# Kernel tuning notes

Measured on AMD Instinct MI355X. Metric: run time of the kernel, lower is better.

Reference implementation:

```python
import jax, jax.numpy as jnp
import numpy as np
import math

# --- delta-LFIT rule-space combinatorics ---
NUM_VARS, DELAYS = 3, 3
N = NUM_VARS * DELAYS  # 9 delayed variables

def delta_count(l, n):
    # number of rule bodies of length exactly l: choose l of n vars, each with a polarity
    return math.comb(n, l) * (2 ** l)

MAX_RULE_LEN = max(delta_count(l, N) for l in range(N + 1))  # 5376
OUT_DIM = MAX_RULE_LEN + 1  # padded logits + trailing 'empty rule' logit
N_HEADS = N + 1  # rules_pred has heads for rule_len = 0..N

B, S = 512, 1
DIM_IN = 1024
DIM_HIDDEN = 1024
LAYERS = 4  # -> LAYERS+1 Linear layers total (no nonlinearity in the original Sequential)


def setup_inputs() -> dict:
    key = jax.random.key(0)
    ks = jax.random.split(key, 4)
    latent = jax.random.normal(ks[0], (B, S, DIM_IN), dtype=jnp.float32)
    rule_len = jax.random.randint(ks[1], (B,), 0, N_HEADS, dtype=jnp.int32)

    n_lin = LAYERS + 1  # dim_in==dim_hidden so all trunk linears stack uniformly
    scale = 1.0 / np.sqrt(DIM_HIDDEN)
    W_mlp = jax.random.normal(ks[2], (n_lin, DIM_HIDDEN, DIM_HIDDEN), dtype=jnp.float32) * scale
    b_mlp = jnp.zeros((n_lin, DIM_HIDDEN), dtype=jnp.float32)

    # Padded head weight bank: row layout matches torch.cat((out[..., :-1], zeros_pad, out[..., -1:]))
    rng = np.random.default_rng(0)
    Wh = np.zeros((N_HEADS, OUT_DIM, DIM_HIDDEN), dtype=np.float32)
    bh = np.zeros((N_HEADS, OUT_DIM), dtype=np.float32)
    for l in range(N_HEADS):
        d = delta_count(l, N) + 1  # head l output dim: length(l)-length(l-1)+1
        w = (rng.standard_normal((d, DIM_HIDDEN)) * scale).astype(np.float32)
        b = (rng.standard_normal(d) * 0.01).astype(np.float32)
        Wh[l, : d - 1] = w[:-1]
        Wh[l, OUT_DIM - 1] = w[-1]
        bh[l, : d - 1] = b[:-1]
        bh[l, OUT_DIM - 1] = b[-1]

    return {
        "latent": latent,
        "W_mlp": W_mlp,
        "b_mlp": b_mlp,
        "W_heads": jnp.asarray(Wh),
        "b_heads": jnp.asarray(bh),
        "rule_len": rule_len,
    }


def reference(latent, W_mlp, b_mlp, W_heads, b_heads, rule_len):
    # Trunk: stack of Linear layers, no activation (matches the original Sequential)
    h = latent  # [B, S, H]
    for i in range(W_mlp.shape[0]):
        h = h @ W_mlp[i].T + b_mlp[i]
    # Per-sample dynamic head dispatch (rule_len_is_diff=True branch), vectorized:
    # compute all padded heads, then gather each sample's head.
    all_out = jnp.einsum('bsh,loh->bslo', h, W_heads) + b_heads  # [B, S, N_HEADS, OUT_DIM]
    idx = rule_len.astype(jnp.int32)[:, None, None, None]  # [B,1,1,1]
    out = jnp.take_along_axis(all_out, idx, axis=2)[:, :, 0, :]  # [B, S, OUT_DIM]
    return out
```

## Files before the change

### kernel.cpp

```cpp
#include <hip/hip_runtime.h>

#define DIM     1024
#define BATCH   512
#define OUTD    5377
#define NHEADS  10
#define NLAYERS 5
#define LDK     72

typedef __attribute__((ext_vector_type(4))) float f32x4;
typedef __attribute__((ext_vector_type(8))) short bf16x8;

__device__ __forceinline__ unsigned short f2bf(float f) {
    unsigned u = __builtin_bit_cast(unsigned, f);
    u = (u + 0x7FFFu + ((u >> 16) & 1u)) >> 16;
    return (unsigned short)u;
}
__device__ __forceinline__ float bf2f(unsigned short h) {
    unsigned u = ((unsigned)h) << 16;
    return __builtin_bit_cast(float, u);
}
__device__ __forceinline__ unsigned pk2(float a, float b) {
    return (unsigned)f2bf(a) | ((unsigned)f2bf(b) << 16);
}

__global__ void group_kernel(const int* __restrict__ rule_len,
                             int* __restrict__ bidx,
                             int* __restrict__ gstart,
                             int* __restrict__ gcount) {
    __shared__ int s_count[NHEADS];
    __shared__ int s_fill[NHEADS];
    int t = threadIdx.x;
    if (t < NHEADS) s_count[t] = 0;
    __syncthreads();
    int h = rule_len[t];
    atomicAdd(&s_count[h], 1);
    __syncthreads();
    if (t == 0) {
        int acc = 0;
        for (int i = 0; i < NHEADS; ++i) {
            gstart[i] = acc;
            gcount[i] = s_count[i];
            s_fill[i] = acc;
            acc += s_count[i];
        }
    }
    __syncthreads();
    int pos = atomicAdd(&s_fill[h], 1);
    bidx[pos] = t;
}

__global__ void convert_latent(const float* __restrict__ in,
                               unsigned short* __restrict__ out) {
    int i = blockIdx.x * blockDim.x + threadIdx.x;
    float4 v = ((const float4*)in)[i];
    ushort4 o;
    o.x = f2bf(v.x); o.y = f2bf(v.y); o.z = f2bf(v.z); o.w = f2bf(v.w);
    ((ushort4*)out)[i] = o;
}

__global__ __launch_bounds__(256) void mlp_mfma(
    const unsigned short* __restrict__ A,
    const float* __restrict__ W,
    const float* __restrict__ bias,
    unsigned short* __restrict__ C)
{
    __shared__ __align__(16) unsigned short As[2][32][LDK];
    __shared__ __align__(16) unsigned short Whi[2][32][LDK];
    __shared__ __align__(16) unsigned short Wlo[2][32][LDK];

    const int tid = threadIdx.x;
    const int n0 = blockIdx.x * 32;
    const int m0 = blockIdx.y * 32;
    const int lane = tid & 63;
    const int wid = tid >> 6;
    const int wm = (wid >> 1) * 16;
    const int wn = (wid & 1) * 16;

    f32x4 acc = {0.f, 0.f, 0.f, 0.f};

    const int ar = tid >> 3;
    const int ac = (tid & 7) * 8;
    const int wr = tid >> 4;
    const int wc = (tid & 15) * 4;

    const unsigned short* Ap = A + (size_t)(m0 + ar) * DIM + ac;
    const float* Wp0 = W + (size_t)(n0 + wr) * DIM + wc;
    const float* Wp1 = W + (size_t)(n0 + wr + 16) * DIM + wc;

    uint4  ra  = *(const uint4*)(Ap);
    float4 rw0 = *(const float4*)(Wp0);
    float4 rw1 = *(const float4*)(Wp1);

    for (int t = 0; t < DIM / 64; ++t) {
        const int cur = t & 1;
        *(uint4*)&As[cur][ar][ac] = ra;
        {
            ushort4 hi, lo;
            hi.x = f2bf(rw0.x); lo.x = f2bf(rw0.x - bf2f(hi.x));
            hi.y = f2bf(rw0.y); lo.y = f2bf(rw0.y - bf2f(hi.y));
            hi.z = f2bf(rw0.z); lo.z = f2bf(rw0.z - bf2f(hi.z));
            hi.w = f2bf(rw0.w); lo.w = f2bf(rw0.w - bf2f(hi.w));
            *(ushort4*)&Whi[cur][wr][wc] = hi;
            *(ushort4*)&Wlo[cur][wr][wc] = lo;
            hi.x = f2bf(rw1.x); lo.x = f2bf(rw1.x - bf2f(hi.x));
            hi.y = f2bf(rw1.y); lo.y = f2bf(rw1.y - bf2f(hi.y));
            hi.z = f2bf(rw1.z); lo.z = f2bf(rw1.z - bf2f(hi.z));
            hi.w = f2bf(rw1.w); lo.w = f2bf(rw1.w - bf2f(hi.w));
            *(ushort4*)&Whi[cur][wr + 16][wc] = hi;
            *(ushort4*)&Wlo[cur][wr + 16][wc] = lo;
        }
        __syncthreads();
        if (t < DIM / 64 - 1) {
            const int k0 = (t + 1) * 64;
            ra  = *(const uint4*)(Ap + k0);
            rw0 = *(const float4*)(Wp0 + k0);
            rw1 = *(const float4*)(Wp1 + k0);
        }
        #pragma unroll
        for (int kk = 0; kk < 2; ++kk) {
            const int ko = kk * 32 + (lane >> 4) * 8;
            bf16x8 a  = *(const bf16x8*)&As[cur][wm + (lane & 15)][ko];
            bf16x8 bh = *(const bf16x8*)&Whi[cur][wn + (lane & 15)][ko];
            bf16x8 bl = *(const bf16x8*)&Wlo[cur][wn + (lane & 15)][ko];
            acc = __builtin_amdgcn_mfma_f32_16x16x32_bf16(a, bh, acc, 0, 0, 0);
            acc = __builtin_amdgcn_mfma_f32_16x16x32_bf16(a, bl, acc, 0, 0, 0);
        }
    }

    const int cn = n0 + wn + (lane & 15);
    const float bn = bias[cn];
    const int rbase = m0 + wm + (lane >> 4) * 4;
    #pragma unroll
    for (int j = 0; j < 4; ++j) {
        C[(size_t)(rbase + j) * DIM + cn] = f2bf(acc[j] + bn);
    }
}

__global__ __launch_bounds__(256, 5) void head_mfma(
    const unsigned short* __restrict__ H,
    const float* __restrict__ Wh,
    const float* __restrict__ bh,
    const int* __restrict__ bidx,
    const int* __restrict__ gstart,
    const int* __restrict__ gcount,
    float* __restrict__ out)
{
    const int head = blockIdx.z;
    const int cnt = gcount[head];
    const int m0 = blockIdx.y * 64;
    if (m0 >= cnt) return;
    const int n0 = blockIdx.x * 32;

    __shared__ __align__(16) unsigned short As[2][64][LDK];
    __shared__ __align__(16) unsigned short Ws[2][32][LDK];
    __shared__ int s_b[64];

    const int tid = threadIdx.x;
    if (tid < 64) {
        int mi = m0 + tid;
        s_b[tid] = (mi < cnt) ? bidx[gstart[head] + mi] : -1;
    }
    __syncthreads();

    const int lane = tid & 63;
    const int wid = tid >> 6;
    const int wm = (wid >> 1) * 32;
    const int wn = (wid & 1) * 16;

    f32x4 acc[2] = {};

    const int ar = tid >> 3;
    const int ac = (tid & 7) * 8;
    int b0 = s_b[ar];       if (b0 < 0) b0 = 0;
    int b1 = s_b[ar + 32];  if (b1 < 0) b1 = 0;
    const unsigned short* Ap0 = H + (size_t)b0 * DIM + ac;
    const unsigned short* Ap1 = H + (size_t)b1 * DIM + ac;

    const int wr = tid >> 3;
    const int wc = (tid & 7) * 8;
    int wrow = n0 + wr; if (wrow > OUTD - 1) wrow = OUTD - 1;
    const float* Wp = Wh + (size_t)head * OUTD * DIM + (size_t)wrow * DIM + wc;

    uint4  pa0[2], pa1[2];
    float4 pw0[2], pw1[2];

    pa0[0] = *(const uint4*)(Ap0);
    pa1[0] = *(const uint4*)(Ap1);
    pw0[0] = *(const float4*)(Wp);
    pw1[0] = *(const float4*)(Wp + 4);
    pa0[1] = *(const uint4*)(Ap0 + 64);
    pa1[1] = *(const uint4*)(Ap1 + 64);
    pw0[1] = *(const float4*)(Wp + 64);
    pw1[1] = *(const float4*)(Wp + 68);

    #pragma unroll
    for (int t = 0; t < DIM / 64; ++t) {
        const int cur = t & 1;
        *(uint4*)&As[cur][ar][ac]      = pa0[cur];
        *(uint4*)&As[cur][ar + 32][ac] = pa1[cur];
        uint4 wp;
        wp.x = pk2(pw0[cur].x, pw0[cur].y);
        wp.y = pk2(pw0[cur].z, pw0[cur].w);
        wp.z = pk2(pw1[cur].x, pw1[cur].y);
        wp.w = pk2(pw1[cur].z, pw1[cur].w);
        *(uint4*)&Ws[cur][wr][wc] = wp;
        asm volatile("s_waitcnt lgkmcnt(0)" ::: "memory");
        __builtin_amdgcn_s_barrier();
        __builtin_amdgcn_sched_barrier(0);
        if (t + 2 < DIM / 64) {
            const int k0 = (t + 2) * 64;
            pa0[cur] = *(const uint4*)(Ap0 + k0);
            pa1[cur] = *(const uint4*)(Ap1 + k0);
            pw0[cur] = *(const float4*)(Wp + k0);
            pw1[cur] = *(const float4*)(Wp + k0 + 4);
        }
        #pragma unroll
        for (int kk = 0; kk < 2; ++kk) {
            const int ko = kk * 32 + (lane >> 4) * 8;
            bf16x8 a0 = *(const bf16x8*)&As[cur][wm + (lane & 15)][ko];
            bf16x8 a1 = *(const bf16x8*)&As[cur][wm + 16 + (lane & 15)][ko];
            bf16x8 w0 = *(const bf16x8*)&Ws[cur][wn + (lane & 15)][ko];
            acc[0] = __builtin_amdgcn_mfma_f32_16x16x32_bf16(a0, w0, acc[0], 0, 0, 0);
            acc[1] = __builtin_amdgcn_mfma_f32_16x16x32_bf16(a1, w0, acc[1], 0, 0, 0);
        }
    }

    const float* bhL = bh + (size_t)head * OUTD;
    const int n = n0 + wn + (lane & 15);
    if (n < OUTD) {
        const float bn = bhL[n];
        #pragma unroll
        for (int fm = 0; fm < 2; ++fm) {
            #pragma unroll
            for (int j = 0; j < 4; ++j) {
                int mi = wm + fm * 16 + (lane >> 4) * 4 + j;
                int b = s_b[mi];
                if (b >= 0) out[(size_t)b * OUTD + n] = acc[fm][j] + bn;
            }
        }
    }
}

extern "C" void kernel_launch(void* const* d_in, const int* in_sizes, int n_in,
                              void* d_out, int out_size, void* d_ws, size_t ws_size,
                              hipStream_t stream) {
    const float* latent   = (const float*)d_in[0];
    const float* W_mlp    = (const float*)d_in[1];
    const float* b_mlp    = (const float*)d_in[2];
    const float* W_heads  = (const float*)d_in[3];
    const float* b_heads  = (const float*)d_in[4];
    const int*   rule_len = (const int*)d_in[5];
    float* out = (float*)d_out;

    unsigned short* h0 = (unsigned short*)d_ws;
    unsigned short* h1 = h0 + (size_t)BATCH * DIM;
    int* bidx   = (int*)(h1 + (size_t)BATCH * DIM);
    int* gstart = bidx + BATCH;
    int* gcount = gstart + 16;

    group_kernel<<<1, BATCH, 0, stream>>>(rule_len, bidx, gstart, gcount);
    convert_latent<<<(BATCH * DIM / 4) / 256, 256, 0, stream>>>(latent, h0);

    dim3 mgrid(DIM / 32, BATCH / 32);
    const unsigned short* src = h0;
    unsigned short* dst = h1;
    for (int l = 0; l < NLAYERS; ++l) {
        mlp_mfma<<<mgrid, 256, 0, stream>>>(src,
                                            W_mlp + (size_t)l * DIM * DIM,
                                            b_mlp + (size_t)l * DIM,
                                            dst);
        unsigned short* t = (unsigned short*)src;
        src = dst;
        dst = t;
    }

    dim3 hgrid((OUTD + 31) / 32, BATCH / 64, NHEADS);
    head_mfma<<<hgrid, 256, 0, stream>>>(src, W_heads, b_heads,
                                         bidx, gstart, gcount, out);
}
```

Before: 127.7 us.

## Replace LDS-tiled head GEMM with register-direct streaming MFMA kernel

The head kernel no longer stages tiles through shared memory with barriers. Each wave now owns 16 output columns and loads fp32 weights and bf16 activations straight from global memory into MFMA operands, covering 64 rows with four accumulators. The block tile grows to 64 columns. This removes LDS traffic and per-tile synchronisation for a weight-bandwidth-bound head, but gives up cross-wave operand sharing. Operand loads become strided per lane (each lane reads 8 contiguous elements of a different row) with no software prefetch, so latency hiding depends on occupancy and unrolling.

After: 191.6 us. 1.5x slower.

```diff
diff --git a/kernel.cpp b/kernel.cpp
--- a/kernel.cpp
+++ b/kernel.cpp
@@ -136,7 +136,7 @@
     }
 }
 
-__global__ __launch_bounds__(256, 5) void head_mfma(
+__global__ __launch_bounds__(256, 4) void head_stream(
     const unsigned short* __restrict__ H,
     const float* __restrict__ Wh,
     const float* __restrict__ bh,
@@ -146,96 +146,63 @@
     float* __restrict__ out)
 {
     const int head = blockIdx.z;
-    const int cnt = gcount[head];
-    const int m0 = blockIdx.y * 64;
+    const int cnt  = gcount[head];
+    const int m0   = blockIdx.y * 64;
     if (m0 >= cnt) return;
-    const int n0 = blockIdx.x * 32;
-
-    __shared__ __align__(16) unsigned short As[2][64][LDK];
-    __shared__ __align__(16) unsigned short Ws[2][32][LDK];
-    __shared__ int s_b[64];
-
-    const int tid = threadIdx.x;
-    if (tid < 64) {
-        int mi = m0 + tid;
-        s_b[tid] = (mi < cnt) ? bidx[gstart[head] + mi] : -1;
-    }
-    __syncthreads();
-
-    const int lane = tid & 63;
-    const int wid = tid >> 6;
-    const int wm = (wid >> 1) * 32;
-    const int wn = (wid & 1) * 16;
-
-    f32x4 acc[2] = {};
-
-    const int ar = tid >> 3;
-    const int ac = (tid & 7) * 8;
-    int b0 = s_b[ar];       if (b0 < 0) b0 = 0;
-    int b1 = s_b[ar + 32];  if (b1 < 0) b1 = 0;
-    const unsigned short* Ap0 = H + (size_t)b0 * DIM + ac;
-    const unsigned short* Ap1 = H + (size_t)b1 * DIM + ac;
-
-    const int wr = tid >> 3;
-    const int wc = (tid & 7) * 8;
-    int wrow = n0 + wr; if (wrow > OUTD - 1) wrow = OUTD - 1;
-    const float* Wp = Wh + (size_t)head * OUTD * DIM + (size_t)wrow * DIM + wc;
-
-    uint4  pa0[2], pa1[2];
-    float4 pw0[2], pw1[2];
-
-    pa0[0] = *(const uint4*)(Ap0);
-    pa1[0] = *(const uint4*)(Ap1);
-    pw0[0] = *(const float4*)(Wp);
-    pw1[0] = *(const float4*)(Wp + 4);
-    pa0[1] = *(const uint4*)(Ap0 + 64);
-    pa1[1] = *(const uint4*)(Ap1 + 64);
-    pw0[1] = *(const float4*)(Wp + 64);
-    pw1[1] = *(const float4*)(Wp + 68);
-
+    const int start = gstart[head];
+
+    const int lane = threadIdx.x & 63;
+    const int wv   = threadIdx.x >> 6;
+    const int n0   = (blockIdx.x * 4 + wv) * 16;
+    const int col  = lane & 15;
+    const int koff = (lane >> 4) * 8;
+
+    int wrow = n0 + col; if (wrow > OUTD - 1) wrow = OUTD - 1;
+    const float* wp = Wh + (size_t)head * OUTD * DIM + (size_t)wrow * DIM + koff;
+
+    const unsigned short* ap[4];
     #pragma unroll
-    for (int t = 0; t < DIM / 64; ++t) {
-        const int cur = t & 1;
-        *(uint4*)&As[cur][ar][ac]      = pa0[cur];
-        *(uint4*)&As[cur][ar + 32][ac] = pa1[cur];
-        uint4 wp;
-        wp.x = pk2(pw0[cur].x, pw0[cur].y);
-        wp.y = pk2(pw0[cur].z, pw0[cur].w);
-        wp.z = pk2(pw1[cur].x, pw1[cur].y);
-        wp.w = pk2(pw1[cur].z, pw1[cur].w);
-        *(uint4*)&Ws[cur][wr][wc] = wp;
-        asm volatile("s_waitcnt lgkmcnt(0)" ::: "memory");
-        __builtin_amdgcn_s_barrier();
-        __builtin_amdgcn_sched_barrier(0);
-        if (t + 2 < DIM / 64) {
-            const int k0 = (t + 2) * 64;
-            pa0[cur] = *(const uint4*)(Ap0 + k0);
-            pa1[cur] = *(const uint4*)(Ap1 + k0);
-            pw0[cur] = *(const float4*)(Wp + k0);
-            pw1[cur] = *(const float4*)(Wp + k0 + 4);
-        }
+    for (int mf = 0; mf < 4; ++mf) {
+        int m = m0 + mf * 16 + col;
+        int idx = (m < cnt) ? m : (cnt - 1);
+        int b = bidx[start + idx];
+        ap[mf] = H + (size_t)b * DIM + koff;
+    }
+
+    f32x4 acc[4] = {};
+
+    #pragma unroll 4
+    for (int eo = 0; eo < DIM; eo += 32) {
+        float4 w0 = *(const float4*)(wp + eo);
+        float4 w1 = *(const float4*)(wp + eo + 4);
+        bf16x8 a0 = *(const bf16x8*)(ap[0] + eo);
+        bf16x8 a1 = *(const bf16x8*)(ap[1] + eo);
+        bf16x8 a2 = *(const bf16x8*)(ap[2] + eo);
+        bf16x8 a3 = *(const bf16x8*)(ap[3] + eo);
+        uint4 wk;
+        wk.x = pk2(w0.x, w0.y);
+        wk.y = pk2(w0.z, w0.w);
+        wk.z = pk2(w1.x, w1.y);
+        wk.w = pk2(w1.z, w1.w);
+        bf16x8 wb = __builtin_bit_cast(bf16x8, wk);
+        acc[0] = __builtin_amdgcn_mfma_f32_16x16x32_bf16(a0, wb, acc[0], 0, 0, 0);
+        acc[1] = __builtin_amdgcn_mfma_f32_16x16x32_bf16(a1, wb, acc[1], 0, 0, 0);
+        acc[2] = __builtin_amdgcn_mfma_f32_16x16x32_bf16(a2, wb, acc[2], 0, 0, 0);
+        acc[3] = __builtin_amdgcn_mfma_f32_16x16x32_bf16(a3, wb, acc[3], 0, 0, 0);
+    }
+
+    const int n = n0 + col;
+    if (n < OUTD) {
+        const float bn = bh[(size_t)head * OUTD + n];
         #pragma unroll
-        for (int kk = 0; kk < 2; ++kk) {
-            const int ko = kk * 32 + (lane >> 4) * 8;
-            bf16x8 a0 = *(const bf16x8*)&As[cur][wm + (lane & 15)][ko];
-            bf16x8 a1 = *(const bf16x8*)&As[cur][wm + 16 + (lane & 15)][ko];
-            bf16x8 w0 = *(const bf16x8*)&Ws[cur][wn + (lane & 15)][ko];
-            acc[0] = __builtin_amdgcn_mfma_f32_16x16x32_bf16(a0, w0, acc[0], 0, 0, 0);
-            acc[1] = __builtin_amdgcn_mfma_f32_16x16x32_bf16(a1, w0, acc[1], 0, 0, 0);
-        }
-    }
-
-    const float* bhL = bh + (size_t)head * OUTD;
-    const int n = n0 + wn + (lane & 15);
-    if (n < OUTD) {
-        const float bn = bhL[n];
-        #pragma unroll
-        for (int fm = 0; fm < 2; ++fm) {
+        for (int mf = 0; mf < 4; ++mf) {
             #pragma unroll
             for (int j = 0; j < 4; ++j) {
-                int mi = wm + fm * 16 + (lane >> 4) * 4 + j;
-                int b = s_b[mi];
-                if (b >= 0) out[(size_t)b * OUTD + n] = acc[fm][j] + bn;
+                int m = m0 + mf * 16 + (lane >> 4) * 4 + j;
+                if (m < cnt) {
+                    int b = bidx[start + m];
+                    out[(size_t)b * OUTD + n] = acc[mf][j] + bn;
+                }
             }
         }
     }
@@ -274,7 +241,7 @@
         dst = t;
     }
 
-    dim3 hgrid((OUTD + 31) / 32, BATCH / 64, NHEADS);
-    head_mfma<<<hgrid, 256, 0, stream>>>(src, W_heads, b_heads,
-                                         bidx, gstart, gcount, out);
-}
+    dim3 hgrid((OUTD + 63) / 64, BATCH / 64, NHEADS);
+    head_stream<<<hgrid, 256, 0, stream>>>(src, W_heads, b_heads,
+                                           bidx, gstart, gcount, out);
+}
```
